# Optimization experiments

Measured on AMD Instinct MI355X. Metric: run time of the kernel, lower is better.

## Reference

```python
import jax, jax.numpy as jnp
import numpy as np

QWEN_H = 2048
SNN_H = 512


def setup_inputs() -> dict:
    key = jax.random.key(0)
    k0, k1, k2, k3, k4 = jax.random.split(key, 5)
    hidden_states = jax.random.normal(k0, (4, 2048, QWEN_H), dtype=jnp.float32)
    # nn.Linear weights stored as [out, in]
    w_down = jax.random.normal(k1, (SNN_H, QWEN_H), dtype=jnp.float32) / np.sqrt(QWEN_H)
    w_up = jax.random.normal(k2, (QWEN_H, SNN_H), dtype=jnp.float32) / np.sqrt(SNN_H)
    w1 = jax.random.normal(k3, (SNN_H, SNN_H), dtype=jnp.float32) / np.sqrt(SNN_H)
    w2 = jax.random.normal(k4, (SNN_H, SNN_H), dtype=jnp.float32) / np.sqrt(SNN_H)
    residual_scale = jnp.float32(0.1)
    return {"hidden_states": hidden_states, "w_down": w_down, "w_up": w_up,
            "w1": w1, "w2": w2, "residual_scale": residual_scale}


def reference(hidden_states, w_down, w_up, w1, w2, residual_scale):
    # Faithful math of SNNMiddleLayer.forward. The spike pulse encode ->
    # SpikeFP32Linear (fp32 accumulation) -> pulse decode path is a lossless
    # FP32 spike encoding of an ordinary bias-free linear layer, so the
    # per-timestep loop computes exactly out_t = w2 @ (w1 @ proj_down(x_t)),
    # which we express as fused batched GEMMs over all timesteps.
    residual = hidden_states
    x = jnp.einsum('bsq,hq->bsh', hidden_states, w_down)   # proj_down
    h = jnp.einsum('bsh,oh->bso', x, w1)                   # snn_linear1
    o = jnp.einsum('bso,po->bsp', h, w2)                   # snn_linear2
    out = jnp.einsum('bsp,qp->bsq', o, w_up)               # proj_up
    return residual + residual_scale * out
```

## Files before the change

### kernel.cpp

```cpp
#include <hip/hip_runtime.h>
#include <hip/hip_bf16.h>
#include <stdint.h>

using bf16 = __hip_bfloat16;
typedef __attribute__((ext_vector_type(8))) short bf16x8;
typedef __attribute__((ext_vector_type(4))) float f32x4;

__device__ __forceinline__ void async_load16(const void* g, void* l) {
    __builtin_amdgcn_global_load_lds(
        (__attribute__((address_space(1))) const void*)g,
        (__attribute__((address_space(3))) void*)l,
        16, 0, 0);
}

__device__ __forceinline__ void cvt_block_2048(const float* __restrict__ src,
                                               bf16* __restrict__ dst, int relblk) {
    int i = (relblk * 256 + (int)threadIdx.x) * 8;
    float4 f0 = *(const float4*)(src + i);
    float4 f1 = *(const float4*)(src + i + 4);
    union { bf16 h[8]; uint4 u; } o;
    o.h[0] = __float2bfloat16(f0.x); o.h[1] = __float2bfloat16(f0.y);
    o.h[2] = __float2bfloat16(f0.z); o.h[3] = __float2bfloat16(f0.w);
    o.h[4] = __float2bfloat16(f1.x); o.h[5] = __float2bfloat16(f1.y);
    o.h[6] = __float2bfloat16(f1.z); o.h[7] = __float2bfloat16(f1.w);
    *(uint4*)(dst + i) = o.u;
}

__global__ __launch_bounds__(256) void cvt3(
    const float* __restrict__ s0, bf16* __restrict__ d0, int nb0,
    const float* __restrict__ s1, bf16* __restrict__ d1, int nb1,
    const float* __restrict__ s2, bf16* __restrict__ d2) {
    int b = blockIdx.x;
    if (b < nb0)            cvt_block_2048(s0, d0, b);
    else if (b < nb0 + nb1) cvt_block_2048(s1, d1, b - nb0);
    else                    cvt_block_2048(s2, d2, b - nb0 - nb1);
}

__global__ __launch_bounds__(256) void cvt_t2(
    const float* __restrict__ s0, bf16* __restrict__ d0, int R0, int C0, int nb0,
    const float* __restrict__ s1, bf16* __restrict__ d1, int R1, int C1) {
    __shared__ bf16 tile[32][33];
    int b = blockIdx.x;
    const float* src; bf16* dst; int R, C, tx, ty;
    if (b < nb0) { src = s0; dst = d0; R = R0; C = C0; int ntx = C0 / 32; tx = b % ntx; ty = b / ntx; }
    else { b -= nb0; src = s1; dst = d1; R = R1; C = C1; int ntx = C1 / 32; tx = b % ntx; ty = b / ntx; }
    const int bx = tx * 32, by = ty * 32;
    const int lx = threadIdx.x & 31;
    const int ly4 = ((int)threadIdx.x >> 5) * 4;
#pragma unroll
    for (int r = 0; r < 4; ++r)
        tile[ly4 + r][lx] = __float2bfloat16(src[(size_t)(by + ly4 + r) * C + bx + lx]);
    __syncthreads();
#pragma unroll
    for (int r = 0; r < 4; ++r)
        dst[(size_t)(bx + ly4 + r) * R + by + lx] = tile[lx][ly4 + r];
}

template<int BN, int EPI>
__global__ __launch_bounds__(256) void gemm_nt(
    const bf16* __restrict__ A, const bf16* __restrict__ B,
    bf16* __restrict__ Cb, float* __restrict__ Cf,
    const float* __restrict__ Res, const float* __restrict__ scale_ptr,
    int M, int N, int K)
{
    constexpr int BM = 128;
    constexpr int NJ = BN / 32;
    __shared__ __align__(16) bf16 As[BM * 32];
    __shared__ __align__(16) bf16 Bs[BN * 32];

    const int tid  = threadIdx.x;
    const int wave = tid >> 6;
    const int lane = tid & 63;
    const int wm = wave >> 1, wn = wave & 1;
    const size_t bm = (size_t)blockIdx.x * BM;
    const size_t bn = (size_t)blockIdx.y * BN;

    f32x4 acc[4][NJ];
#pragma unroll
    for (int i = 0; i < 4; ++i)
#pragma unroll
        for (int j = 0; j < NJ; ++j)
            acc[i][j] = (f32x4){0.f, 0.f, 0.f, 0.f};

    const int srow = lane >> 2;
    const int scol = (lane & 3) * 8;

    for (int k0 = 0; k0 < K; k0 += 32) {
#pragma unroll
        for (int c = 0; c < (BM + BN) / 64; ++c) {
            const int rbase = c * 64 + wave * 16;
            if (rbase < BM)
                async_load16(A + (bm + rbase + srow) * (size_t)K + k0 + scol, &As[rbase * 32]);
            else
                async_load16(B + (bn + (rbase - BM) + srow) * (size_t)K + k0 + scol,
                             &Bs[(rbase - BM) * 32]);
        }
        __syncthreads();

        bf16x8 af[4], bfr[NJ];
#pragma unroll
        for (int i = 0; i < 4; ++i)
            af[i] = *(const bf16x8*)&As[(wm * 64 + i * 16 + (lane & 15)) * 32 + (lane >> 4) * 8];
#pragma unroll
        for (int j = 0; j < NJ; ++j)
            bfr[j] = *(const bf16x8*)&Bs[(wn * (BN / 2) + j * 16 + (lane & 15)) * 32 + (lane >> 4) * 8];
#pragma unroll
        for (int i = 0; i < 4; ++i)
#pragma unroll
            for (int j = 0; j < NJ; ++j)
                acc[i][j] = __builtin_amdgcn_mfma_f32_16x16x32_bf16(af[i], bfr[j], acc[i][j], 0, 0, 0);
        __syncthreads();
    }

    const int col_l = lane & 15;
    const int row_l = (lane >> 4) * 4;
    if (EPI == 0) {
#pragma unroll
        for (int i = 0; i < 4; ++i)
#pragma unroll
            for (int j = 0; j < NJ; ++j)
#pragma unroll
                for (int r = 0; r < 4; ++r) {
                    size_t row = bm + wm * 64 + i * 16 + row_l + r;
                    size_t col = bn + wn * (BN / 2) + j * 16 + col_l;
                    Cb[row * (size_t)N + col] = __float2bfloat16(acc[i][j][r]);
                }
    } else {
        const float s = *scale_ptr;
#pragma unroll
        for (int i = 0; i < 4; ++i)
#pragma unroll
            for (int j = 0; j < NJ; ++j)
#pragma unroll
                for (int r = 0; r < 4; ++r) {
                    size_t row = bm + wm * 64 + i * 16 + row_l + r;
                    size_t col = bn + wn * (BN / 2) + j * 16 + col_l;
                    size_t idx = row * (size_t)N + col;
                    Cf[idx] = Res[idx] + s * acc[i][j][r];
                }
    }
}

extern "C" void kernel_launch(void* const* d_in, const int* in_sizes, int n_in,
                              void* d_out, int out_size, void* d_ws, size_t ws_size,
                              hipStream_t stream) {
    const float* hs     = (const float*)d_in[0];
    const float* w_down = (const float*)d_in[1];
    const float* w_up   = (const float*)d_in[2];
    const float* w1     = (const float*)d_in[3];
    const float* w2     = (const float*)d_in[4];
    const float* rs     = (const float*)d_in[5];

    const int T = 8192, Q = 2048, H = 512;

    char* ws = (char*)d_ws;
    bf16* hs_b  = (bf16*)(ws + 0);
    bf16* x_b   = (bf16*)(ws + 33554432);
    bf16* w1_b  = (bf16*)(ws + 41943040);
    bf16* wu_b  = (bf16*)(ws + 42467328);
    bf16* wdt_b = (bf16*)(ws + 44564480);
    bf16* w2t_b = (bf16*)(ws + 46661632);
    bf16* Rm    = (bf16*)(ws + 47185920);
    bf16* Um    = (bf16*)(ws + 49283072);

    cvt3<<<dim3(8192 + 128 + 512), dim3(256), 0, stream>>>(hs, hs_b, 8192, w1, w1_b, 128, w_up, wu_b);
    cvt_t2<<<dim3(1024 + 256), dim3(256), 0, stream>>>(w_down, wdt_b, H, Q, 1024, w2, w2t_b, H, H);

    dim3 blk(256);
    gemm_nt<64, 0><<<dim3(H / 128, Q / 64), blk, 0, stream>>>(w1_b, wdt_b, Rm, nullptr, nullptr, nullptr, H, Q, H);
    gemm_nt<64, 0><<<dim3(Q / 128, H / 64), blk, 0, stream>>>(wu_b, w2t_b, Um, nullptr, nullptr, nullptr, Q, H, H);
    gemm_nt<64, 0><<<dim3(T / 128, H / 64), blk, 0, stream>>>(hs_b, Rm, x_b, nullptr, nullptr, nullptr, T, H, Q);
    gemm_nt<128, 1><<<dim3(T / 128, Q / 128), blk, 0, stream>>>(x_b, Um, nullptr, (float*)d_out, hs, rs, T, Q, H);
}
```

Baseline: 221.2 us.

## Fuse fp32 hidden-state conversion into GEMM, widen K tile, swizzle LDS, merge launches

Removes the separate pass that converted the large fp32 hidden_states tensor to bf16. The down-projection GEMM now loads fp32 rows and converts them to bf16 in registers before storing to LDS. The K tile grows from 32 to 64 with an XOR-swizzled LDS layout to reduce bank conflicts. The weight-prep kernels are merged into one launch, the two small weight-product GEMMs share a single launch, and the grid axes are swapped so N varies fastest. In exchange, the fp32 A path uses synchronous global loads instead of async LDS loads, and each block reloads its A rows for every N tile.

```diff
diff --git a/kernel.cpp b/kernel.cpp
--- a/kernel.cpp
+++ b/kernel.cpp
@@ -26,54 +26,51 @@
     *(uint4*)(dst + i) = o.u;
 }
 
-__global__ __launch_bounds__(256) void cvt3(
-    const float* __restrict__ s0, bf16* __restrict__ d0, int nb0,
-    const float* __restrict__ s1, bf16* __restrict__ d1, int nb1,
-    const float* __restrict__ s2, bf16* __restrict__ d2) {
-    int b = blockIdx.x;
-    if (b < nb0)            cvt_block_2048(s0, d0, b);
-    else if (b < nb0 + nb1) cvt_block_2048(s1, d1, b - nb0);
-    else                    cvt_block_2048(s2, d2, b - nb0 - nb1);
-}
-
-__global__ __launch_bounds__(256) void cvt_t2(
-    const float* __restrict__ s0, bf16* __restrict__ d0, int R0, int C0, int nb0,
-    const float* __restrict__ s1, bf16* __restrict__ d1, int R1, int C1) {
-    __shared__ bf16 tile[32][33];
-    int b = blockIdx.x;
-    const float* src; bf16* dst; int R, C, tx, ty;
-    if (b < nb0) { src = s0; dst = d0; R = R0; C = C0; int ntx = C0 / 32; tx = b % ntx; ty = b / ntx; }
-    else { b -= nb0; src = s1; dst = d1; R = R1; C = C1; int ntx = C1 / 32; tx = b % ntx; ty = b / ntx; }
-    const int bx = tx * 32, by = ty * 32;
+__device__ __forceinline__ void transp_tile(const float* __restrict__ src,
+                                            bf16* __restrict__ dst, int R, int C,
+                                            int tile, int ntx, bf16 (*sh)[33]) {
+    const int bx = (tile % ntx) * 32, by = (tile / ntx) * 32;
     const int lx = threadIdx.x & 31;
     const int ly4 = ((int)threadIdx.x >> 5) * 4;
 #pragma unroll
     for (int r = 0; r < 4; ++r)
-        tile[ly4 + r][lx] = __float2bfloat16(src[(size_t)(by + ly4 + r) * C + bx + lx]);
+        sh[ly4 + r][lx] = __float2bfloat16(src[(size_t)(by + ly4 + r) * C + bx + lx]);
     __syncthreads();
 #pragma unroll
     for (int r = 0; r < 4; ++r)
-        dst[(size_t)(bx + ly4 + r) * R + by + lx] = tile[lx][ly4 + r];
-}
-
-template<int BN, int EPI>
-__global__ __launch_bounds__(256) void gemm_nt(
-    const bf16* __restrict__ A, const bf16* __restrict__ B,
+        dst[(size_t)(bx + ly4 + r) * R + by + lx] = sh[lx][ly4 + r];
+}
+
+__global__ __launch_bounds__(256) void prep(
+    const float* __restrict__ w1, bf16* __restrict__ w1b,
+    const float* __restrict__ wup, bf16* __restrict__ wub,
+    const float* __restrict__ wd, bf16* __restrict__ wdt,
+    const float* __restrict__ w2, bf16* __restrict__ w2t) {
+    __shared__ bf16 sh[32][33];
+    int b = blockIdx.x;
+    if (b < 128)        cvt_block_2048(w1, w1b, b);
+    else if (b < 640)   cvt_block_2048(wup, wub, b - 128);
+    else if (b < 1664)  transp_tile(wd, wdt, 512, 2048, b - 640, 64, sh);
+    else                transp_tile(w2, w2t, 512, 512, b - 1664, 16, sh);
+}
+
+template<int BN, int EPI, bool AFP32>
+__device__ __forceinline__ void gemm_core(
+    const void* __restrict__ Aptr, const bf16* __restrict__ B,
     bf16* __restrict__ Cb, float* __restrict__ Cf,
-    const float* __restrict__ Res, const float* __restrict__ scale_ptr,
-    int M, int N, int K)
+    const float* __restrict__ Res, const float* __restrict__ sp,
+    int N, int K, int bxi, int byi, bf16* As, bf16* Bs)
 {
     constexpr int BM = 128;
     constexpr int NJ = BN / 32;
-    __shared__ __align__(16) bf16 As[BM * 32];
-    __shared__ __align__(16) bf16 Bs[BN * 32];
+    static_assert(BN == 64 || BN == 128, "BN");
 
     const int tid  = threadIdx.x;
     const int wave = tid >> 6;
     const int lane = tid & 63;
     const int wm = wave >> 1, wn = wave & 1;
-    const size_t bm = (size_t)blockIdx.x * BM;
-    const size_t bn = (size_t)blockIdx.y * BN;
+    const size_t bm = (size_t)bxi * BM;
+    const size_t bn = (size_t)byi * BN;
 
     f32x4 acc[4][NJ];
 #pragma unroll
@@ -82,33 +79,79 @@
         for (int j = 0; j < NJ; ++j)
             acc[i][j] = (f32x4){0.f, 0.f, 0.f, 0.f};
 
-    const int srow = lane >> 2;
-    const int scol = (lane & 3) * 8;
-
-    for (int k0 = 0; k0 < K; k0 += 32) {
-#pragma unroll
-        for (int c = 0; c < (BM + BN) / 64; ++c) {
-            const int rbase = c * 64 + wave * 16;
-            if (rbase < BM)
-                async_load16(A + (bm + rbase + srow) * (size_t)K + k0 + scol, &As[rbase * 32]);
-            else
-                async_load16(B + (bn + (rbase - BM) + srow) * (size_t)K + k0 + scol,
-                             &Bs[(rbase - BM) * 32]);
+    const int srow  = lane >> 3;
+    const int scol8 = (lane & 7) ^ srow;
+    const int arow = tid >> 2;
+    const int aq   = tid & 3;
+
+    for (int k0 = 0; k0 < K; k0 += 64) {
+        if (AFP32) {
+            const float* Af = (const float*)Aptr;
+#pragma unroll
+            for (int p = 0; p < 2; ++p) {
+                const int row = p * 64 + arow;
+                const float* s = Af + (bm + row) * (size_t)K + k0 + aq * 16;
+                float4 f0 = *(const float4*)(s);
+                float4 f1 = *(const float4*)(s + 4);
+                float4 f2 = *(const float4*)(s + 8);
+                float4 f3 = *(const float4*)(s + 12);
+                union { bf16 h[8]; uint4 u; } o0, o1;
+                o0.h[0] = __float2bfloat16(f0.x); o0.h[1] = __float2bfloat16(f0.y);
+                o0.h[2] = __float2bfloat16(f0.z); o0.h[3] = __float2bfloat16(f0.w);
+                o0.h[4] = __float2bfloat16(f1.x); o0.h[5] = __float2bfloat16(f1.y);
+                o0.h[6] = __float2bfloat16(f1.z); o0.h[7] = __float2bfloat16(f1.w);
+                o1.h[0] = __float2bfloat16(f2.x); o1.h[1] = __float2bfloat16(f2.y);
+                o1.h[2] = __float2bfloat16(f2.z); o1.h[3] = __float2bfloat16(f2.w);
+                o1.h[4] = __float2bfloat16(f3.x); o1.h[5] = __float2bfloat16(f3.y);
+                o1.h[6] = __float2bfloat16(f3.z); o1.h[7] = __float2bfloat16(f3.w);
+                const int r7 = row & 7;
+                *(uint4*)&As[(size_t)(row * 8 + ((2 * aq) ^ r7)) * 8]     = o0.u;
+                *(uint4*)&As[(size_t)(row * 8 + ((2 * aq + 1) ^ r7)) * 8] = o1.u;
+            }
+#pragma unroll
+            for (int c = 0; c < BN / 32; ++c) {
+                const int cc = wave + c * 4;
+                const int rb = cc * 8;
+                async_load16(B + (bn + rb + srow) * (size_t)K + k0 + scol8 * 8, &Bs[rb * 64]);
+            }
+        } else {
+            const bf16* Ab = (const bf16*)Aptr;
+            constexpr int TOT = (BM + BN) / 8;
+#pragma unroll
+            for (int c = 0; c < TOT / 4; ++c) {
+                const int cc = wave + c * 4;
+                if (cc < BM / 8) {
+                    const int rb = cc * 8;
+                    async_load16(Ab + (bm + rb + srow) * (size_t)K + k0 + scol8 * 8, &As[rb * 64]);
+                } else {
+                    const int rb = (cc - BM / 8) * 8;
+                    async_load16(B + (bn + rb + srow) * (size_t)K + k0 + scol8 * 8, &Bs[rb * 64]);
+                }
+            }
         }
         __syncthreads();
 
-        bf16x8 af[4], bfr[NJ];
-#pragma unroll
-        for (int i = 0; i < 4; ++i)
-            af[i] = *(const bf16x8*)&As[(wm * 64 + i * 16 + (lane & 15)) * 32 + (lane >> 4) * 8];
-#pragma unroll
-        for (int j = 0; j < NJ; ++j)
-            bfr[j] = *(const bf16x8*)&Bs[(wn * (BN / 2) + j * 16 + (lane & 15)) * 32 + (lane >> 4) * 8];
-#pragma unroll
-        for (int i = 0; i < 4; ++i)
-#pragma unroll
-            for (int j = 0; j < NJ; ++j)
-                acc[i][j] = __builtin_amdgcn_mfma_f32_16x16x32_bf16(af[i], bfr[j], acc[i][j], 0, 0, 0);
+#pragma unroll
+        for (int kk = 0; kk < 2; ++kk) {
+            bf16x8 af[4], bfr[NJ];
+#pragma unroll
+            for (int i = 0; i < 4; ++i) {
+                const int r  = wm * 64 + i * 16 + (lane & 15);
+                const int c8 = kk * 4 + (lane >> 4);
+                af[i] = *(const bf16x8*)&As[(size_t)(r * 8 + (c8 ^ (r & 7))) * 8];
+            }
+#pragma unroll
+            for (int j = 0; j < NJ; ++j) {
+                const int r  = wn * (BN / 2) + j * 16 + (lane & 15);
+                const int c8 = kk * 4 + (lane >> 4);
+                bfr[j] = *(const bf16x8*)&Bs[(size_t)(r * 8 + (c8 ^ (r & 7))) * 8];
+            }
+#pragma unroll
+            for (int i = 0; i < 4; ++i)
+#pragma unroll
+                for (int j = 0; j < NJ; ++j)
+                    acc[i][j] = __builtin_amdgcn_mfma_f32_16x16x32_bf16(af[i], bfr[j], acc[i][j], 0, 0, 0);
+        }
         __syncthreads();
     }
 
@@ -126,7 +169,7 @@
                     Cb[row * (size_t)N + col] = __float2bfloat16(acc[i][j][r]);
                 }
     } else {
-        const float s = *scale_ptr;
+        const float s = *sp;
 #pragma unroll
         for (int i = 0; i < 4; ++i)
 #pragma unroll
@@ -138,6 +181,42 @@
                     size_t idx = row * (size_t)N + col;
                     Cf[idx] = Res[idx] + s * acc[i][j][r];
                 }
+    }
+}
+
+template<int BN, int EPI>
+__global__ __launch_bounds__(256) void gemm_bf16(
+    const bf16* __restrict__ A, const bf16* __restrict__ B,
+    bf16* __restrict__ Cb, float* __restrict__ Cf,
+    const float* __restrict__ Res, const float* __restrict__ sp, int N, int K) {
+    __shared__ __align__(16) bf16 As[128 * 64];
+    __shared__ __align__(16) bf16 Bs[BN * 64];
+    gemm_core<BN, EPI, false>(A, B, Cb, Cf, Res, sp, N, K, blockIdx.y, blockIdx.x, As, Bs);
+}
+
+__global__ __launch_bounds__(256) void gemm_xf32(
+    const float* __restrict__ A, const bf16* __restrict__ B,
+    bf16* __restrict__ Cb, int N, int K) {
+    __shared__ __align__(16) bf16 As[128 * 64];
+    __shared__ __align__(16) bf16 Bs[64 * 64];
+    gemm_core<64, 0, true>(A, B, Cb, nullptr, nullptr, nullptr, N, K, blockIdx.y, blockIdx.x, As, Bs);
+}
+
+__global__ __launch_bounds__(256) void gemm_ru(
+    const bf16* __restrict__ A0, const bf16* __restrict__ B0, bf16* __restrict__ C0,
+    int N0, int K0, int nb0, int nt0,
+    const bf16* __restrict__ A1, const bf16* __restrict__ B1, bf16* __restrict__ C1,
+    int N1, int K1, int nt1) {
+    __shared__ __align__(16) bf16 As[128 * 64];
+    __shared__ __align__(16) bf16 Bs[64 * 64];
+    int b = blockIdx.x;
+    if (b < nb0)
+        gemm_core<64, 0, false>(A0, B0, C0, nullptr, nullptr, nullptr, N0, K0,
+                                b / nt0, b % nt0, As, Bs);
+    else {
+        b -= nb0;
+        gemm_core<64, 0, false>(A1, B1, C1, nullptr, nullptr, nullptr, N1, K1,
+                                b / nt1, b % nt1, As, Bs);
     }
 }
 
@@ -151,24 +230,19 @@
     const float* w2     = (const float*)d_in[4];
     const float* rs     = (const float*)d_in[5];
 
-    const int T = 8192, Q = 2048, H = 512;
-
     char* ws = (char*)d_ws;
-    bf16* hs_b  = (bf16*)(ws + 0);
-    bf16* x_b   = (bf16*)(ws + 33554432);
-    bf16* w1_b  = (bf16*)(ws + 41943040);
-    bf16* wu_b  = (bf16*)(ws + 42467328);
-    bf16* wdt_b = (bf16*)(ws + 44564480);
-    bf16* w2t_b = (bf16*)(ws + 46661632);
-    bf16* Rm    = (bf16*)(ws + 47185920);
-    bf16* Um    = (bf16*)(ws + 49283072);
-
-    cvt3<<<dim3(8192 + 128 + 512), dim3(256), 0, stream>>>(hs, hs_b, 8192, w1, w1_b, 128, w_up, wu_b);
-    cvt_t2<<<dim3(1024 + 256), dim3(256), 0, stream>>>(w_down, wdt_b, H, Q, 1024, w2, w2t_b, H, H);
-
-    dim3 blk(256);
-    gemm_nt<64, 0><<<dim3(H / 128, Q / 64), blk, 0, stream>>>(w1_b, wdt_b, Rm, nullptr, nullptr, nullptr, H, Q, H);
-    gemm_nt<64, 0><<<dim3(Q / 128, H / 64), blk, 0, stream>>>(wu_b, w2t_b, Um, nullptr, nullptr, nullptr, Q, H, H);
-    gemm_nt<64, 0><<<dim3(T / 128, H / 64), blk, 0, stream>>>(hs_b, Rm, x_b, nullptr, nullptr, nullptr, T, H, Q);
-    gemm_nt<128, 1><<<dim3(T / 128, Q / 128), blk, 0, stream>>>(x_b, Um, nullptr, (float*)d_out, hs, rs, T, Q, H);
-}
+    bf16* x_b   = (bf16*)(ws + 0);
+    bf16* w1_b  = (bf16*)(ws + 8388608);
+    bf16* wu_b  = (bf16*)(ws + 8912896);
+    bf16* wdt_b = (bf16*)(ws + 11010048);
+    bf16* w2t_b = (bf16*)(ws + 13107200);
+    bf16* Rm    = (bf16*)(ws + 13631488);
+    bf16* Um    = (bf16*)(ws + 15728640);
+
+    prep<<<dim3(1920), dim3(256), 0, stream>>>(w1, w1_b, w_up, wu_b, w_down, wdt_b, w2, w2t_b);
+    gemm_ru<<<dim3(256), dim3(256), 0, stream>>>(w1_b, wdt_b, Rm, 2048, 512, 128, 32,
+                                                 wu_b, w2t_b, Um, 512, 512, 8);
+    gemm_xf32<<<dim3(8, 64), dim3(256), 0, stream>>>(hs, Rm, x_b, 512, 2048);
+    gemm_bf16<128, 1><<<dim3(16, 64), dim3(256), 0, stream>>>(x_b, Um, nullptr, (float*)d_out,
+                                                              hs, rs, 2048, 512);
+}
```

Result: slower. 232.2 us (+5.0%).
